# Kernel tuning notes

Hardware: AMD Instinct MI355X
Metric: run time of the kernel (lower is better)

## Reference

```python
import jax, jax.numpy as jnp
import numpy as np

U = 50000
I = 50000
N = U + I
D = 128
T = 3
L = 2
E = 3200000
B = 4096


def setup_inputs() -> dict:
    key = jax.random.key(0)
    ks = jax.random.split(key, 20)
    xav = lambda k, shp: jax.random.normal(k, shp, jnp.float32) * (2.0 / (shp[0] + shp[-1])) ** 0.5
    return {
        'user_indices': jax.random.randint(ks[0], (B,), 0, U, jnp.int32),
        'item_indices': jax.random.randint(ks[1], (B,), 0, I, jnp.int32),
        'edge_index': jax.random.randint(ks[2], (2, E), 0, N, jnp.int32),
        'adj_values': jax.random.uniform(ks[3], (E,), jnp.float32),
        'user_table': jax.random.normal(ks[4], (U, D), jnp.float32) * 0.01,
        'item_table': jax.random.normal(ks[5], (I, D), jnp.float32) * 0.01,
        'temporal_emb': xav(ks[6], (T, D)),
        'gcn_w': jnp.stack([xav(ks[7 + l], (D, D)) for l in range(L)]),
        'gcn_b': jnp.zeros((L, D), jnp.float32),
        'att_w1': xav(ks[9], (2 * D, D)), 'att_b1': jnp.zeros((D,), jnp.float32),
        'att_w2': xav(ks[10], (D, T)), 'att_b2': jnp.zeros((T,), jnp.float32),
        'pred_w1': xav(ks[11], (2 * D, D)), 'pred_b1': jnp.zeros((D,), jnp.float32),
        'pred_w2': xav(ks[12], (D, 1)), 'pred_b2': jnp.zeros((1,), jnp.float32),
    }


def _spmm(edge_index, adj_values, s):
    # A @ s with COO adjacency: gather src rows, scale, scatter-add to dst rows
    msgs = adj_values[:, None] * s[edge_index[1]]  # [E, D]
    return jax.ops.segment_sum(msgs, edge_index[0], num_segments=N)


def reference(user_indices, item_indices, edge_index, adj_values, user_table,
              item_table, temporal_emb, gcn_w, gcn_b, att_w1, att_b1, att_w2,
              att_b2, pred_w1, pred_b1, pred_w2, pred_b2):
    user_emb = user_table[user_indices]          # [B, D]
    item_emb = item_table[item_indices]          # [B, D]
    x = jnp.concatenate([user_table, item_table], axis=0)  # [N, D]

    temporal_outs = []
    for t in range(T):
        h = x + temporal_emb[t]
        for l in range(L):
            support = h @ gcn_w[l]
            h = jax.nn.relu(_spmm(edge_index, adj_values, support) + gcn_b[l])
        bu = h[:U][user_indices]                 # [B, D]
        bi = h[U:][item_indices]                 # [B, D]
        temporal_outs.append(jnp.concatenate([bu, bi], axis=1))
    temporal_stack = jnp.stack(temporal_outs, axis=1)  # [B, T, 2D]

    concat_orig = jnp.concatenate([user_emb, item_emb], axis=1)  # [B, 2D]
    att_h = jax.nn.relu(concat_orig @ att_w1 + att_b1)
    attn = jax.nn.softmax(att_h @ att_w2 + att_b2, axis=1)       # [B, T]
    summed = jnp.sum(temporal_stack * attn[:, :, None], axis=1)  # [B, 2D]

    ph = jax.nn.relu(summed @ pred_w1 + pred_b1)  # dropout in eval mode: identity
    pred = ph @ pred_w2 + pred_b2                 # [B, 1]
    return pred.squeeze(-1)
```

## Files before the change

kernel.cpp:

```cpp
#include <hip/hip_runtime.h>

#define U_CNT 50000
#define I_CNT 50000
#define N_NODES 100000
#define DD 128
#define T_STEPS 3
#define E_CNT 3200000
#define B_SZ 4096

#define NCOARSE 391
#define NBLK_BIN 256
#define CHUNK ((E_CNT + NBLK_BIN - 1) / NBLK_BIN)
#define SORT_CAP 10240
#define S_SCALE 256.0f
#define S_INV (1.0f / 256.0f)
#define VQ 32767.0f
#define VQ_INV (1.0f / 32767.0f)
#define FB 8

typedef float v2f __attribute__((ext_vector_type(2)));
typedef short bf16x8 __attribute__((ext_vector_type(8)));
typedef float f32x4 __attribute__((ext_vector_type(4)));

__device__ __forceinline__ float bf2f(unsigned short u) {
    return __uint_as_float(((unsigned int)u) << 16);
}
__device__ __forceinline__ unsigned short f2bf(float f) {
    unsigned int x = __float_as_uint(f);
    x += 0x7FFF + ((x >> 16) & 1);
    return (unsigned short)(x >> 16);
}

__global__ void __launch_bounds__(256) k_bin_count(const int* __restrict__ dst,
                                                   int* __restrict__ hist) {
    __shared__ int c[NCOARSE];
    int blk = blockIdx.x, tid = threadIdx.x;
    for (int j = tid; j < NCOARSE; j += 256) c[j] = 0;
    __syncthreads();
    int s0 = blk * CHUNK, s1 = min(E_CNT, s0 + CHUNK);
    for (int i = s0 + tid; i < s1; i += 256)
        atomicAdd(&c[__builtin_nontemporal_load(&dst[i]) >> 8], 1);
    __syncthreads();
    for (int j = tid; j < NCOARSE; j += 256) hist[blk * NCOARSE + j] = c[j];
}

__global__ void __launch_bounds__(512) k_scan_a(const int* __restrict__ hist,
                                                int* __restrict__ exact_base,
                                                int* __restrict__ row_ptr) {
    __shared__ int tot[NCOARSE];
    int tid = threadIdx.x;
    for (int b = tid; b < NCOARSE; b += 512) {
        int s = 0;
        for (int blk = 0; blk < NBLK_BIN; ++blk) s += hist[blk * NCOARSE + b];
        tot[b] = s;
    }
    __syncthreads();
    if (tid == 0) {
        int run = 0;
        for (int b = 0; b < NCOARSE; ++b) {
            exact_base[b] = run;
            run += tot[b];
        }
        exact_base[NCOARSE] = run;
        row_ptr[N_NODES] = run;
    }
}

__global__ void __launch_bounds__(NBLK_BIN) k_scan_b(int* __restrict__ hist,
                                                     const int* __restrict__ exact_base) {
    __shared__ int lds[NBLK_BIN];
    int b = blockIdx.x, tid = threadIdx.x;
    int v = hist[tid * NCOARSE + b];
    lds[tid] = v;
    __syncthreads();
    for (int off = 1; off < NBLK_BIN; off <<= 1) {
        int add = (tid >= off) ? lds[tid - off] : 0;
        __syncthreads();
        lds[tid] += add;
        __syncthreads();
    }
    hist[tid * NCOARSE + b] = exact_base[b] + lds[tid] - v;
}

__global__ void __launch_bounds__(256) k_bin_scatter(const int* __restrict__ dst,
                                                     const int* __restrict__ src,
                                                     const float* __restrict__ val,
                                                     const int* __restrict__ blkbase,
                                                     int2* __restrict__ binned) {
    __shared__ int cur[NCOARSE];
    int blk = blockIdx.x, tid = threadIdx.x;
    for (int b = tid; b < NCOARSE; b += 256) cur[b] = blkbase[blk * NCOARSE + b];
    __syncthreads();
    int s0 = blk * CHUNK, s1 = min(E_CNT, s0 + CHUNK);
    for (int i = s0 + tid; i < s1; i += 256) {
        int d = __builtin_nontemporal_load(&dst[i]);
        int s = __builtin_nontemporal_load(&src[i]);
        float w = __builtin_nontemporal_load(&val[i]);
        int b = d >> 8;
        int pos = atomicAdd(&cur[b], 1);
        binned[pos] = make_int2(s | ((d & 255) << 20), __float_as_int(w));
    }
}

__global__ void __launch_bounds__(256) k_sort(const int* __restrict__ exact_base,
                                              const int2* __restrict__ binned,
                                              unsigned int* __restrict__ outp,
                                              int* __restrict__ row_ptr) {
    __shared__ int hist[256], scn[256], cur[256];
    __shared__ unsigned short perm[SORT_CAP];
    int b = blockIdx.x, tid = threadIdx.x;
    int ebase = exact_base[b];
    int cnt = exact_base[b + 1] - ebase;
    if (cnt > SORT_CAP) cnt = SORT_CAP;
    const int2* rbase = binned + ebase;
    int n0 = b << 8;
    hist[tid] = 0;
    __syncthreads();
    for (int i = tid; i < cnt; i += 256) atomicAdd(&hist[(rbase[i].x >> 20) & 255], 1);
    __syncthreads();
    scn[tid] = hist[tid];
    __syncthreads();
    for (int off = 1; off < 256; off <<= 1) {
        int v = (tid >= off) ? scn[tid - off] : 0;
        __syncthreads();
        scn[tid] += v;
        __syncthreads();
    }
    int excl = scn[tid] - hist[tid];
    cur[tid] = excl;
    if (n0 + tid < N_NODES) row_ptr[n0 + tid] = ebase + excl;
    __syncthreads();
    for (int i = tid; i < cnt; i += 256) {
        int dloc = (rbase[i].x >> 20) & 255;
        int pos = atomicAdd(&cur[dloc], 1);
        perm[pos] = (unsigned short)i;
    }
    __syncthreads();
    for (int i = tid; i < cnt; i += 256) {
        int2 p = rbase[perm[i]];
        unsigned vq = (unsigned)(__int_as_float(p.y) * VQ + 0.5f);
        outp[ebase + i] = (vq << 17) | (unsigned)(p.x & 0x1FFFF);
    }
}

__global__ void k_uvec(const float* __restrict__ temb, const float* __restrict__ w0,
                       float* __restrict__ u) {
    int k = threadIdx.x;
    for (int t = 0; t < T_STEPS; ++t) {
        float acc = 0.f;
        for (int j = 0; j < DD; ++j) acc += temb[t * DD + j] * w0[j * DD + k];
        u[t * DD + k] = acc;
    }
}

__global__ void __launch_bounds__(256) k_gemm0(const float* __restrict__ utab,
                                               const float* __restrict__ itab,
                                               const float* __restrict__ W,
                                               unsigned char* __restrict__ outf8) {
    __shared__ unsigned short wfrag[8][4][64][8];
    __shared__ unsigned short xs[64 * 128];
    int tid = threadIdx.x;
    #pragma unroll
    for (int ii = 0; ii < 16; ++ii) {
        int idx = tid * 64 + ii * 4;
        int k = idx >> 7, n0 = idx & 127;
        float4 w4 = *reinterpret_cast<const float4*>(&W[idx]);
        int s = k >> 5, kb = (k >> 3) & 3, j = k & 7;
        float wv[4] = {w4.x, w4.y, w4.z, w4.w};
        #pragma unroll
        for (int m = 0; m < 4; ++m) {
            int n = n0 + m;
            wfrag[n >> 4][s][(n & 15) | (kb << 4)][j] = f2bf(wv[m]);
        }
    }
    int lane = tid & 63, wid = tid >> 6;
    const int ntiles = (N_NODES + 63) / 64;
    for (int tile = blockIdx.x; tile < ntiles; tile += gridDim.x) {
        __syncthreads();
        int tbase = tile * 64;
        #pragma unroll
        for (int p = 0; p < 8; ++p) {
            int idx = p * 1024 + tid * 4;
            int row = idx >> 7, c = idx & 127;
            int grow = tbase + row;
            float4 a = make_float4(0.f, 0.f, 0.f, 0.f);
            if (grow < N_NODES) {
                const float* src = (grow < U_CNT) ? &utab[(size_t)grow * DD + c]
                                                  : &itab[(size_t)(grow - U_CNT) * DD + c];
                a = *reinterpret_cast<const float4*>(src);
            }
            int si = (row * 128 + c) ^ ((row & 7) << 3);
            ushort4 o = {f2bf(a.x), f2bf(a.y), f2bf(a.z), f2bf(a.w)};
            *reinterpret_cast<ushort4*>(&xs[si]) = o;
        }
        __syncthreads();
        int rowt = wid * 16 + (lane & 15);
        int kb = lane >> 4;
        bf16x8 afrag[4];
        #pragma unroll
        for (int s = 0; s < 4; ++s) {
            int si = (rowt * 128 + s * 32 + kb * 8) ^ ((rowt & 7) << 3);
            afrag[s] = *reinterpret_cast<bf16x8*>(&xs[si]);
        }
        int wbase = tbase + wid * 16;
        #pragma unroll
        for (int c = 0; c < 8; ++c) {
            f32x4 acc = {0.f, 0.f, 0.f, 0.f};
            #pragma unroll
            for (int s = 0; s < 4; ++s) {
                bf16x8 bfrag = *reinterpret_cast<bf16x8*>(&wfrag[c][s][lane][0]);
                acc = __builtin_amdgcn_mfma_f32_16x16x32_bf16(afrag[s], bfrag, acc, 0, 0, 0);
            }
            int orow0 = wbase + (lane >> 4) * 4;
            int ocol = c * 16 + (lane & 15);
            #pragma unroll
            for (int r = 0; r < 4; ++r) {
                int orow = orow0 + r;
                if (orow < N_NODES) {
                    unsigned pk = __builtin_amdgcn_cvt_pk_fp8_f32(acc[r] * S_SCALE,
                                                                  acc[r] * S_SCALE, 0, false);
                    outf8[(size_t)orow * DD + ocol] = (unsigned char)(pk & 0xFF);
                }
            }
        }
    }
}

__global__ void __launch_bounds__(256) k_spmm_full(const int* __restrict__ row_ptr,
                                                   const unsigned int* __restrict__ pack,
                                                   const unsigned char* __restrict__ Sf,
                                                   unsigned short* __restrict__ Pb,
                                                   float* __restrict__ rvec) {
    int wave = (int)((blockIdx.x * blockDim.x + threadIdx.x) >> 6);
    int lane = threadIdx.x & 63;
    if (wave >= N_NODES) return;
    int beg = row_ptr[wave], end = row_ptr[wave + 1];
    int q = lane >> 3;
    int cg = lane & 7;
    v2f acc[8];
    #pragma unroll
    for (int j = 0; j < 8; ++j) acc[j] = (v2f){0.f, 0.f};
    float vs = 0.f;
    int e0 = beg + q;
    unsigned pl = (e0 < end) ? __builtin_nontemporal_load(&pack[e0]) : 0u;
    for (int e = beg; e < end; e += 8) {
        unsigned cur = pl;
        int en = e + 8 + q;
        pl = (en < end) ? __builtin_nontemporal_load(&pack[en]) : 0u;
        int sx = (int)(cur & 0x1FFFF);
        float v = (float)(cur >> 17) * VQ_INV;
        const int4 s4 = *reinterpret_cast<const int4*>(&Sf[((size_t)sx << 7) + (cg << 4)]);
        v2f vv = {v, v};
        acc[0] += vv * __builtin_amdgcn_cvt_pk_f32_fp8(s4.x, false);
        acc[1] += vv * __builtin_amdgcn_cvt_pk_f32_fp8(s4.x, true);
        acc[2] += vv * __builtin_amdgcn_cvt_pk_f32_fp8(s4.y, false);
        acc[3] += vv * __builtin_amdgcn_cvt_pk_f32_fp8(s4.y, true);
        acc[4] += vv * __builtin_amdgcn_cvt_pk_f32_fp8(s4.z, false);
        acc[5] += vv * __builtin_amdgcn_cvt_pk_f32_fp8(s4.z, true);
        acc[6] += vv * __builtin_amdgcn_cvt_pk_f32_fp8(s4.w, false);
        acc[7] += vv * __builtin_amdgcn_cvt_pk_f32_fp8(s4.w, true);
        if (cg == 0) vs += v;
    }
    float out[16];
    #pragma unroll
    for (int j = 0; j < 8; ++j) {
        out[2 * j] = acc[j].x;
        out[2 * j + 1] = acc[j].y;
    }
    #pragma unroll
    for (int j = 0; j < 16; ++j) {
        out[j] += __shfl_down(out[j], 32, 64);
        out[j] += __shfl_down(out[j], 16, 64);
        out[j] += __shfl_down(out[j], 8, 64);
        out[j] *= S_INV;
    }
    vs += __shfl_down(vs, 32, 64);
    vs += __shfl_down(vs, 16, 64);
    vs += __shfl_down(vs, 8, 64);
    if (lane < 8) {
        unsigned w0 = ((unsigned)f2bf(out[1]) << 16) | f2bf(out[0]);
        unsigned w1 = ((unsigned)f2bf(out[3]) << 16) | f2bf(out[2]);
        unsigned w2 = ((unsigned)f2bf(out[5]) << 16) | f2bf(out[4]);
        unsigned w3 = ((unsigned)f2bf(out[7]) << 16) | f2bf(out[6]);
        unsigned w4 = ((unsigned)f2bf(out[9]) << 16) | f2bf(out[8]);
        unsigned w5 = ((unsigned)f2bf(out[11]) << 16) | f2bf(out[10]);
        unsigned w6 = ((unsigned)f2bf(out[13]) << 16) | f2bf(out[12]);
        unsigned w7 = ((unsigned)f2bf(out[15]) << 16) | f2bf(out[14]);
        unsigned short* base = &Pb[((size_t)wave << 7) + (lane << 4)];
        *reinterpret_cast<int4*>(base) = make_int4(w0, w1, w2, w3);
        *reinterpret_cast<int4*>(base + 8) = make_int4(w4, w5, w6, w7);
        if (lane == 0) rvec[wave] = vs;
    }
}

__global__ void __launch_bounds__(256) k_spmm_out3(const int* __restrict__ row_ptr,
                                                   const unsigned int* __restrict__ pack,
                                                   const unsigned short* __restrict__ Pb,
                                                   const float* __restrict__ rvec,
                                                   const int* __restrict__ uidx,
                                                   const int* __restrict__ iidx,
                                                   const float* __restrict__ uvec,
                                                   const float* __restrict__ b0,
                                                   float* __restrict__ agg) {
    int slot = (int)((blockIdx.x * blockDim.x + threadIdx.x) >> 6);
    int lane = threadIdx.x & 63;
    if (slot >= 2 * B_SZ) return;
    int b = slot & (B_SZ - 1), side = slot >> 12;
    int row = side ? (U_CNT + iidx[b]) : uidx[b];
    int beg = row_ptr[row], end = row_ptr[row + 1];
    int half = lane >> 5, cg = lane & 31;
    float u0[4], u1[4], u2[4], bb[4];
    #pragma unroll
    for (int j = 0; j < 4; ++j) {
        int c = cg * 4 + j;
        u0[j] = uvec[c];
        u1[j] = uvec[DD + c];
        u2[j] = uvec[2 * DD + c];
        bb[j] = b0[c];
    }
    float a0[4] = {0, 0, 0, 0}, a1[4] = {0, 0, 0, 0}, a2[4] = {0, 0, 0, 0};
    for (int e = beg; e < end; e += 2) {
        int ee = e + half;
        unsigned pw = (ee < end) ? __builtin_nontemporal_load(&pack[ee]) : 0u;
        int sx = (int)(pw & 0x1FFFF);
        float v = (float)(pw >> 17) * VQ_INV;
        float rr = rvec[sx];
        ushort4 s4 = *reinterpret_cast<const ushort4*>(&Pb[(size_t)sx * DD + cg * 4]);
        float pc[4] = {bf2f(s4.x), bf2f(s4.y), bf2f(s4.z), bf2f(s4.w)};
        #pragma unroll
        for (int j = 0; j < 4; ++j) {
            float base = pc[j] + bb[j];
            a0[j] += v * fmaxf(base + rr * u0[j], 0.f);
            a1[j] += v * fmaxf(base + rr * u1[j], 0.f);
            a2[j] += v * fmaxf(base + rr * u2[j], 0.f);
        }
    }
    #pragma unroll
    for (int j = 0; j < 4; ++j) {
        a0[j] += __shfl_down(a0[j], 32, 64);
        a1[j] += __shfl_down(a1[j], 32, 64);
        a2[j] += __shfl_down(a2[j], 32, 64);
    }
    if (lane < 32) {
        size_t rb = (size_t)slot * 3;
        float4 o0 = {a0[0], a0[1], a0[2], a0[3]};
        float4 o1 = {a1[0], a1[1], a1[2], a1[3]};
        float4 o2 = {a2[0], a2[1], a2[2], a2[3]};
        *reinterpret_cast<float4*>(&agg[(rb + 0) * DD + lane * 4]) = o0;
        *reinterpret_cast<float4*>(&agg[(rb + 1) * DD + lane * 4]) = o1;
        *reinterpret_cast<float4*>(&agg[(rb + 2) * DD + lane * 4]) = o2;
    }
}

__global__ void __launch_bounds__(256) k_head(const float* __restrict__ agg,
                                              const float* __restrict__ W,
                                              const float* __restrict__ b1,
                                              float* __restrict__ tstack) {
    __shared__ unsigned short wfrag[8][4][64][8];
    __shared__ unsigned short xs[64 * 128];
    __shared__ float blds[DD];
    int tid = threadIdx.x;
    #pragma unroll
    for (int ii = 0; ii < 16; ++ii) {
        int idx = tid * 64 + ii * 4;
        int k = idx >> 7, n0 = idx & 127;
        float4 w4 = *reinterpret_cast<const float4*>(&W[idx]);
        int s = k >> 5, kb = (k >> 3) & 3, j = k & 7;
        float wv[4] = {w4.x, w4.y, w4.z, w4.w};
        #pragma unroll
        for (int m = 0; m < 4; ++m) {
            int n = n0 + m;
            wfrag[n >> 4][s][(n & 15) | (kb << 4)][j] = f2bf(wv[m]);
        }
    }
    if (tid < DD) blds[tid] = b1[tid];
    int lane = tid & 63, wid = tid >> 6;
    const int NR = 2 * B_SZ * T_STEPS;
    const int ntiles = NR / 64;
    for (int tile = blockIdx.x; tile < ntiles; tile += gridDim.x) {
        __syncthreads();
        int tbase = tile * 64;
        #pragma unroll
        for (int p = 0; p < 8; ++p) {
            int idx = p * 1024 + tid * 4;
            int row = idx >> 7, c = idx & 127;
            float4 a = *reinterpret_cast<const float4*>(&agg[(size_t)(tbase + row) * DD + c]);
            int si = (row * 128 + c) ^ ((row & 7) << 3);
            ushort4 o = {f2bf(a.x), f2bf(a.y), f2bf(a.z), f2bf(a.w)};
            *reinterpret_cast<ushort4*>(&xs[si]) = o;
        }
        __syncthreads();
        int rowt = wid * 16 + (lane & 15);
        int kb = lane >> 4;
        bf16x8 afrag[4];
        #pragma unroll
        for (int s = 0; s < 4; ++s) {
            int si = (rowt * 128 + s * 32 + kb * 8) ^ ((rowt & 7) << 3);
            afrag[s] = *reinterpret_cast<bf16x8*>(&xs[si]);
        }
        int wbase = tbase + wid * 16;
        #pragma unroll
        for (int c = 0; c < 8; ++c) {
            f32x4 acc = {0.f, 0.f, 0.f, 0.f};
            #pragma unroll
            for (int s = 0; s < 4; ++s) {
                bf16x8 bfrag = *reinterpret_cast<bf16x8*>(&wfrag[c][s][lane][0]);
                acc = __builtin_amdgcn_mfma_f32_16x16x32_bf16(afrag[s], bfrag, acc, 0, 0, 0);
            }
            int orow0 = wbase + (lane >> 4) * 4;
            int ocol = c * 16 + (lane & 15);
            float bb = blds[ocol];
            #pragma unroll
            for (int r = 0; r < 4; ++r) {
                int orow = orow0 + r;
                int slot = orow / 3, t = orow - slot * 3;
                int bi = slot & (B_SZ - 1), side = slot >> 12;
                float o = fmaxf(acc[r] + bb, 0.f);
                tstack[((size_t)bi * T_STEPS + t) * 2 * DD + side * DD + ocol] = o;
            }
        }
    }
}

__global__ void __launch_bounds__(256) k_final(const int* __restrict__ uidx,
                                               const int* __restrict__ iidx,
                                               const float* __restrict__ utab,
                                               const float* __restrict__ itab,
                                               const float* __restrict__ aw1,
                                               const float* __restrict__ ab1,
                                               const float* __restrict__ aw2,
                                               const float* __restrict__ ab2,
                                               const float* __restrict__ pw1,
                                               const float* __restrict__ pb1,
                                               const float* __restrict__ pw2,
                                               const float* __restrict__ pb2,
                                               const float* __restrict__ tstack,
                                               float* __restrict__ outp) {
    __shared__ float s[FB][2 * DD];
    __shared__ float ah[FB][DD];
    __shared__ float attn[FB][4];
    __shared__ float summed[FB][2 * DD];
    __shared__ float red[FB][DD];
    __shared__ int uu[FB], ii[FB];
    int b0 = blockIdx.x * FB, tid = threadIdx.x;
    if (tid < FB) {
        uu[tid] = uidx[b0 + tid];
        ii[tid] = iidx[b0 + tid];
    }
    __syncthreads();
    #pragma unroll
    for (int r = 0; r < FB; ++r)
        s[r][tid] = (tid < DD) ? utab[(size_t)uu[r] * DD + tid]
                               : itab[(size_t)ii[r] * DD + (tid - DD)];
    __syncthreads();
    {
        int c = tid & 127, g = tid >> 7;
        float acc0 = ab1[c], acc1 = acc0, acc2 = acc0, acc3 = acc0;
        for (int k = 0; k < 2 * DD; ++k) {
            float w = aw1[k * DD + c];
            acc0 += s[g][k] * w;
            acc1 += s[g + 2][k] * w;
            acc2 += s[g + 4][k] * w;
            acc3 += s[g + 6][k] * w;
        }
        ah[g][c] = fmaxf(acc0, 0.f);
        ah[g + 2][c] = fmaxf(acc1, 0.f);
        ah[g + 4][c] = fmaxf(acc2, 0.f);
        ah[g + 6][c] = fmaxf(acc3, 0.f);
    }
    __syncthreads();
    if (tid < FB * T_STEPS) {
        int r = tid / 3, t = tid - r * 3;
        float lg = ab2[t];
        for (int k = 0; k < DD; ++k) lg += ah[r][k] * aw2[k * T_STEPS + t];
        attn[r][t] = lg;
    }
    __syncthreads();
    if (tid < FB) {
        float m = fmaxf(attn[tid][0], fmaxf(attn[tid][1], attn[tid][2]));
        float e0 = expf(attn[tid][0] - m), e1 = expf(attn[tid][1] - m),
              e2 = expf(attn[tid][2] - m);
        float inv = 1.f / (e0 + e1 + e2);
        attn[tid][0] = e0 * inv;
        attn[tid][1] = e1 * inv;
        attn[tid][2] = e2 * inv;
    }
    __syncthreads();
    #pragma unroll
    for (int r = 0; r < FB; ++r) {
        const float* tb = &tstack[(size_t)(b0 + r) * T_STEPS * 2 * DD];
        summed[r][tid] =
            attn[r][0] * tb[tid] + attn[r][1] * tb[2 * DD + tid] + attn[r][2] * tb[4 * DD + tid];
    }
    __syncthreads();
    {
        int c = tid & 127, g = tid >> 7;
        float p0 = pb1[c], p1 = p0, p2 = p0, p3 = p0;
        for (int k = 0; k < 2 * DD; ++k) {
            float w = pw1[k * DD + c];
            p0 += summed[g][k] * w;
            p1 += summed[g + 2][k] * w;
            p2 += summed[g + 4][k] * w;
            p3 += summed[g + 6][k] * w;
        }
        float wc = pw2[c];
        red[g][c] = fmaxf(p0, 0.f) * wc;
        red[g + 2][c] = fmaxf(p1, 0.f) * wc;
        red[g + 4][c] = fmaxf(p2, 0.f) * wc;
        red[g + 6][c] = fmaxf(p3, 0.f) * wc;
    }
    __syncthreads();
    if (tid < FB) {
        float sum = pb2[0];
        for (int k = 0; k < DD; ++k) sum += red[tid][k];
        outp[b0 + tid] = sum;
    }
}

extern "C" void kernel_launch(void* const* d_in, const int* in_sizes, int n_in,
                              void* d_out, int out_size, void* d_ws, size_t ws_size,
                              hipStream_t stream) {
    const int* uidx = (const int*)d_in[0];
    const int* iidx = (const int*)d_in[1];
    const int* eidx = (const int*)d_in[2];
    const float* adj = (const float*)d_in[3];
    const float* utab = (const float*)d_in[4];
    const float* itab = (const float*)d_in[5];
    const float* temb = (const float*)d_in[6];
    const float* gw = (const float*)d_in[7];
    const float* gb = (const float*)d_in[8];
    const float* aw1 = (const float*)d_in[9];
    const float* ab1 = (const float*)d_in[10];
    const float* aw2 = (const float*)d_in[11];
    const float* ab2 = (const float*)d_in[12];
    const float* pw1 = (const float*)d_in[13];
    const float* pb1 = (const float*)d_in[14];
    const float* pw2 = (const float*)d_in[15];
    const float* pb2 = (const float*)d_in[16];

    char* ws = (char*)d_ws;
    size_t off = 0;
    auto alloc = [&](size_t bytes) {
        void* p = ws + off;
        off += (bytes + 255) & ~(size_t)255;
        return p;
    };
    int* hist = (int*)alloc((size_t)NBLK_BIN * NCOARSE * 4);
    int* exact_base = (int*)alloc((NCOARSE + 1) * 4);
    int* row_ptr = (int*)alloc((size_t)(N_NODES + 1) * 4);
    unsigned int* sorted = (unsigned int*)alloc((size_t)E_CNT * 4);
    float* rvec = (float*)alloc((size_t)N_NODES * 4);
    float* uvec = (float*)alloc((size_t)T_STEPS * DD * 4);
    void* un = alloc((size_t)E_CNT * 8);
    int2* binned = (int2*)un;
    unsigned char* Sf = (unsigned char*)un;
    unsigned short* Pb = (unsigned short*)alloc((size_t)N_NODES * DD * 2);
    float* agg = (float*)alloc((size_t)2 * B_SZ * T_STEPS * DD * 4);
    float* tstack = (float*)alloc((size_t)B_SZ * T_STEPS * 2 * DD * 4);

    k_bin_count<<<NBLK_BIN, 256, 0, stream>>>(eidx, hist);
    k_scan_a<<<1, 512, 0, stream>>>(hist, exact_base, row_ptr);
    k_scan_b<<<NCOARSE, NBLK_BIN, 0, stream>>>(hist, exact_base);
    k_bin_scatter<<<NBLK_BIN, 256, 0, stream>>>(eidx, eidx + E_CNT, adj, hist, binned);
    k_sort<<<NCOARSE, 256, 0, stream>>>(exact_base, binned, sorted, row_ptr);
    k_gemm0<<<512, 256, 0, stream>>>(utab, itab, gw, Sf);
    k_uvec<<<1, DD, 0, stream>>>(temb, gw, uvec);
    k_spmm_full<<<(N_NODES + 3) / 4, 256, 0, stream>>>(row_ptr, sorted, Sf, Pb, rvec);
    k_spmm_out3<<<(2 * B_SZ * 64) / 256, 256, 0, stream>>>(row_ptr, sorted, Pb, rvec,
                                                           uidx, iidx, uvec, gb, agg);
    k_head<<<384, 256, 0, stream>>>(agg, gw + DD * DD, gb + DD, tstack);
    k_final<<<B_SZ / FB, 256, 0, stream>>>(uidx, iidx, utab, itab, aw1, ab1, aw2, ab2,
                                           pw1, pb1, pw2, pb2, tstack, (float*)d_out);
}
```

Measured before the change: 303.7 us.

## Use finer 128-row bins, stage sort in LDS, and prefetch gathers in SpMM

Shrinks the coarse bins from 256 to 128 destination rows, doubling the bin count and the number of binning blocks. The sort kernel now stages each bin's edges in LDS and scatters them directly to their final positions, replacing the perm array and the second global re-read. The SpMM loop software-pipelines the fp8 row gather one edge-group ahead so memory latency overlaps the FMA work. This costs more LDS per sort block and more registers in SpMM, and bins larger than the smaller SORT_CAP would be truncated.

```diff
diff --git a/kernel.cpp b/kernel.cpp
--- a/kernel.cpp
+++ b/kernel.cpp
@@ -8,10 +8,12 @@
 #define E_CNT 3200000
 #define B_SZ 4096
 
-#define NCOARSE 391
-#define NBLK_BIN 256
+#define BSHIFT 7
+#define BROWS 128
+#define NCOARSE 782
+#define NBLK_BIN 512
 #define CHUNK ((E_CNT + NBLK_BIN - 1) / NBLK_BIN)
-#define SORT_CAP 10240
+#define SORT_CAP 6144
 #define S_SCALE 256.0f
 #define S_INV (1.0f / 256.0f)
 #define VQ 32767.0f
@@ -39,7 +41,7 @@
     __syncthreads();
     int s0 = blk * CHUNK, s1 = min(E_CNT, s0 + CHUNK);
     for (int i = s0 + tid; i < s1; i += 256)
-        atomicAdd(&c[__builtin_nontemporal_load(&dst[i]) >> 8], 1);
+        atomicAdd(&c[__builtin_nontemporal_load(&dst[i]) >> BSHIFT], 1);
     __syncthreads();
     for (int j = tid; j < NCOARSE; j += 256) hist[blk * NCOARSE + j] = c[j];
 }
@@ -96,9 +98,9 @@
         int d = __builtin_nontemporal_load(&dst[i]);
         int s = __builtin_nontemporal_load(&src[i]);
         float w = __builtin_nontemporal_load(&val[i]);
-        int b = d >> 8;
+        int b = d >> BSHIFT;
         int pos = atomicAdd(&cur[b], 1);
-        binned[pos] = make_int2(s | ((d & 255) << 20), __float_as_int(w));
+        binned[pos] = make_int2(s | ((d & (BROWS - 1)) << 20), __float_as_int(w));
     }
 }
 
@@ -106,40 +108,43 @@
                                               const int2* __restrict__ binned,
                                               unsigned int* __restrict__ outp,
                                               int* __restrict__ row_ptr) {
-    __shared__ int hist[256], scn[256], cur[256];
-    __shared__ unsigned short perm[SORT_CAP];
+    __shared__ int hist[BROWS], scn[BROWS], cur[BROWS];
+    __shared__ int2 stage[SORT_CAP];
     int b = blockIdx.x, tid = threadIdx.x;
     int ebase = exact_base[b];
     int cnt = exact_base[b + 1] - ebase;
     if (cnt > SORT_CAP) cnt = SORT_CAP;
     const int2* rbase = binned + ebase;
-    int n0 = b << 8;
-    hist[tid] = 0;
-    __syncthreads();
-    for (int i = tid; i < cnt; i += 256) atomicAdd(&hist[(rbase[i].x >> 20) & 255], 1);
-    __syncthreads();
-    scn[tid] = hist[tid];
-    __syncthreads();
-    for (int off = 1; off < 256; off <<= 1) {
-        int v = (tid >= off) ? scn[tid - off] : 0;
-        __syncthreads();
-        scn[tid] += v;
-        __syncthreads();
-    }
-    int excl = scn[tid] - hist[tid];
-    cur[tid] = excl;
-    if (n0 + tid < N_NODES) row_ptr[n0 + tid] = ebase + excl;
+    int n0 = b << BSHIFT;
+    if (tid < BROWS) hist[tid] = 0;
     __syncthreads();
     for (int i = tid; i < cnt; i += 256) {
-        int dloc = (rbase[i].x >> 20) & 255;
+        int2 p = rbase[i];
+        stage[i] = p;
+        atomicAdd(&hist[(p.x >> 20) & (BROWS - 1)], 1);
+    }
+    __syncthreads();
+    if (tid < BROWS) scn[tid] = hist[tid];
+    __syncthreads();
+    for (int off = 1; off < BROWS; off <<= 1) {
+        int v = 0;
+        if (tid < BROWS && tid >= off) v = scn[tid - off];
+        __syncthreads();
+        if (tid < BROWS) scn[tid] += v;
+        __syncthreads();
+    }
+    if (tid < BROWS) {
+        int excl = scn[tid] - hist[tid];
+        cur[tid] = excl;
+        if (n0 + tid < N_NODES) row_ptr[n0 + tid] = ebase + excl;
+    }
+    __syncthreads();
+    for (int i = tid; i < cnt; i += 256) {
+        int2 p = stage[i];
+        int dloc = (p.x >> 20) & (BROWS - 1);
         int pos = atomicAdd(&cur[dloc], 1);
-        perm[pos] = (unsigned short)i;
-    }
-    __syncthreads();
-    for (int i = tid; i < cnt; i += 256) {
-        int2 p = rbase[perm[i]];
         unsigned vq = (unsigned)(__int_as_float(p.y) * VQ + 0.5f);
-        outp[ebase + i] = (vq << 17) | (unsigned)(p.x & 0x1FFFF);
+        outp[ebase + pos] = (vq << 17) | (unsigned)(p.x & 0x1FFFF);
     }
 }
 
@@ -242,24 +247,34 @@
     for (int j = 0; j < 8; ++j) acc[j] = (v2f){0.f, 0.f};
     float vs = 0.f;
     int e0 = beg + q;
-    unsigned pl = (e0 < end) ? __builtin_nontemporal_load(&pack[e0]) : 0u;
+    unsigned pl0 = (e0 < end) ? __builtin_nontemporal_load(&pack[e0]) : 0u;
+    int4 s_cur = make_int4(0, 0, 0, 0);
+    if (beg < end)
+        s_cur = *reinterpret_cast<const int4*>(&Sf[((size_t)(pl0 & 0x1FFFF) << 7) + (cg << 4)]);
+    float v_cur = (float)(pl0 >> 17) * VQ_INV;
+    unsigned pl_next = (e0 + 8 < end) ? __builtin_nontemporal_load(&pack[e0 + 8]) : 0u;
     for (int e = beg; e < end; e += 8) {
-        unsigned cur = pl;
-        int en = e + 8 + q;
-        pl = (en < end) ? __builtin_nontemporal_load(&pack[en]) : 0u;
-        int sx = (int)(cur & 0x1FFFF);
-        float v = (float)(cur >> 17) * VQ_INV;
-        const int4 s4 = *reinterpret_cast<const int4*>(&Sf[((size_t)sx << 7) + (cg << 4)]);
-        v2f vv = {v, v};
-        acc[0] += vv * __builtin_amdgcn_cvt_pk_f32_fp8(s4.x, false);
-        acc[1] += vv * __builtin_amdgcn_cvt_pk_f32_fp8(s4.x, true);
-        acc[2] += vv * __builtin_amdgcn_cvt_pk_f32_fp8(s4.y, false);
-        acc[3] += vv * __builtin_amdgcn_cvt_pk_f32_fp8(s4.y, true);
-        acc[4] += vv * __builtin_amdgcn_cvt_pk_f32_fp8(s4.z, false);
-        acc[5] += vv * __builtin_amdgcn_cvt_pk_f32_fp8(s4.z, true);
-        acc[6] += vv * __builtin_amdgcn_cvt_pk_f32_fp8(s4.w, false);
-        acc[7] += vv * __builtin_amdgcn_cvt_pk_f32_fp8(s4.w, true);
-        if (cg == 0) vs += v;
+        bool more = (e + 8 < end);
+        int4 s_next = make_int4(0, 0, 0, 0);
+        if (more)
+            s_next = *reinterpret_cast<const int4*>(
+                &Sf[((size_t)(pl_next & 0x1FFFF) << 7) + (cg << 4)]);
+        float v_n = (float)(pl_next >> 17) * VQ_INV;
+        int e2 = e + 16 + q;
+        unsigned pl2 = (e2 < end) ? __builtin_nontemporal_load(&pack[e2]) : 0u;
+        v2f vv = {v_cur, v_cur};
+        acc[0] += vv * __builtin_amdgcn_cvt_pk_f32_fp8(s_cur.x, false);
+        acc[1] += vv * __builtin_amdgcn_cvt_pk_f32_fp8(s_cur.x, true);
+        acc[2] += vv * __builtin_amdgcn_cvt_pk_f32_fp8(s_cur.y, false);
+        acc[3] += vv * __builtin_amdgcn_cvt_pk_f32_fp8(s_cur.y, true);
+        acc[4] += vv * __builtin_amdgcn_cvt_pk_f32_fp8(s_cur.z, false);
+        acc[5] += vv * __builtin_amdgcn_cvt_pk_f32_fp8(s_cur.z, true);
+        acc[6] += vv * __builtin_amdgcn_cvt_pk_f32_fp8(s_cur.w, false);
+        acc[7] += vv * __builtin_amdgcn_cvt_pk_f32_fp8(s_cur.w, true);
+        if (cg == 0) vs += v_cur;
+        s_cur = s_next;
+        v_cur = v_n;
+        pl_next = pl2;
     }
     float out[16];
     #pragma unroll
```

Result: slower. 334.5 us (+10.1%).
